# Kernel tuning notes

Hardware: AMD Instinct MI355X
Metric: run time of the kernel (lower is better)

Reference implementation:

```python
import jax, jax.numpy as jnp
import numpy as np

EPS = 1e-12
N_HEADS = 16


def _ln(x, g, b, eps=EPS):
    m = jnp.mean(x, axis=-1, keepdims=True)
    v = jnp.var(x, axis=-1, keepdims=True)
    return (x - m) * jax.lax.rsqrt(v + eps) * g + b


def setup_inputs() -> dict:
    key = jax.random.key(0)
    ks = jax.random.split(key, 8)
    B, S, D, I = 2, 2048, 1024, 4096
    s = 0.02
    f32 = jnp.float32
    return {
        "x": jax.random.normal(ks[0], (B, S, D), f32),
        "input_mask": jnp.zeros((B, 1, 1, S), f32),  # additive mask, 0 = no masking
        "norm_w": jnp.ones((D,), f32),
        "norm_b": jnp.zeros((D,), f32),
        "attn_qkvw": jax.random.normal(ks[1], (D, 3 * D), f32) * s,
        "attn_qkvb": jnp.zeros((3 * D,), f32),
        "attn_ow": jax.random.normal(ks[2], (D, D), f32) * s,
        "attn_ob": jnp.zeros((D,), f32),
        "attn_nw": jnp.ones((D,), f32),
        "attn_nb": jnp.zeros((D,), f32),
        "inter_w": jax.random.normal(ks[3], (D, I), f32) * s,
        "inter_b": jnp.zeros((I,), f32),
        "inter_w1": jax.random.normal(ks[4], (D, I), f32) * s,
        "output_w": jax.random.normal(ks[5], (I, D), f32) * s,
        "output_b": jnp.zeros((D,), f32),
    }


def reference(x, input_mask, norm_w, norm_b, attn_qkvw, attn_qkvb, attn_ow,
              attn_ob, attn_nw, attn_nb, inter_w, inter_b, inter_w1,
              output_w, output_b):
    B, S, D = x.shape
    hd = D // N_HEADS

    # --- fused qkv_gemm: pre-layernorm + QKV GEMM + bias ---
    ln1 = _ln(x, norm_w, norm_b)
    qkv = ln1 @ attn_qkvw + attn_qkvb            # [B,S,3D]
    q, k, v = jnp.split(qkv, 3, axis=-1)

    def to_heads(t):  # [B,S,D] -> [B,H,S,hd]
        return t.reshape(B, S, N_HEADS, hd).transpose(0, 2, 1, 3)

    q, k, v = to_heads(q), to_heads(k), to_heads(v)

    # --- softmax-context attention (scale_attention=True -> 1/sqrt(head_dim)) ---
    scores = jnp.einsum('bhqd,bhkd->bhqk', q, k) / jnp.sqrt(jnp.float32(hd))
    scores = scores + input_mask                 # additive mask [B,1,1,S]
    probs = jax.nn.softmax(scores, axis=-1)
    ctx = jnp.einsum('bhqk,bhkd->bhqd', probs, v)
    ctx = ctx.transpose(0, 2, 1, 3).reshape(B, S, D)

    attn_out = ctx @ attn_ow                     # vector_matmul (no bias)

    # --- fused mlp_gemm: bias+residual add, layernorm, GEMM+bias+gelu ---
    residual_add = attn_out + attn_ob + x
    ln2 = _ln(residual_add, attn_nw, attn_nb)
    intermediate = jax.nn.gelu(ln2 @ inter_w + inter_b, approximate=False)
    # gated path: vector_matmul(mlp input, inter_w1) * intermediate (per source)
    intermediate = (attn_out @ inter_w1) * intermediate

    # --- output projection + bias_residual ---
    out = intermediate @ output_w + output_b + residual_add
    return out
```

## Files before the change

kernel.cpp:

```cpp
#include <hip/hip_runtime.h>
#include <hip/hip_bf16.h>

#define BATCH 2
#define SEQ   2048
#define DIM   1024
#define IDIM  4096
#define NH    16
#define HD    64
#define TOK   (BATCH * SEQ)

typedef __hip_bfloat16 bf16;

typedef short bf16x8_t __attribute__((ext_vector_type(8)));
typedef float f32x4_t  __attribute__((ext_vector_type(4)));

__device__ __forceinline__ float ldv(const float* p, size_t i) { return p[i]; }
__device__ __forceinline__ float ldv(const bf16*  p, size_t i) { return __bfloat162float(p[i]); }
__device__ __forceinline__ void  stv(float* p, size_t i, float v) { p[i] = v; }
__device__ __forceinline__ void  stv(bf16*  p, size_t i, float v) { p[i] = __float2bfloat16(v); }

__device__ __forceinline__ f32x4_t mfma16(bf16x8_t a, bf16x8_t b, f32x4_t c) {
    return __builtin_amdgcn_mfma_f32_16x16x32_bf16(a, b, c, 0, 0, 0);
}

__device__ __forceinline__ void gload16(const bf16* g, bf16* l) {
    __builtin_amdgcn_global_load_lds(
        (const __attribute__((address_space(1))) void*)g,
        (__attribute__((address_space(3))) void*)l, 16, 0, 0);
}

__device__ __forceinline__ void xcd_map(int &bx, int &by) {
    const int gn  = gridDim.x;
    const int lin = blockIdx.y * gn + blockIdx.x;
    const int cx  = gn >> 3;
    const int xcd = lin & 7;
    const int slot = lin >> 3;
    bx = xcd * cx + slot % cx;
    by = slot / cx;
}

__device__ __forceinline__ void ln_one_row(const float* __restrict__ in,
                                           const float* __restrict__ w,
                                           const float* __restrict__ b,
                                           bf16* __restrict__ out,
                                           int row, int lane) {
    const float4* xr = (const float4*)(in + (size_t)row * DIM);
    float4 v[4];
    float sum = 0.f, sq = 0.f;
#pragma unroll
    for (int i = 0; i < 4; i++) {
        v[i] = xr[lane + i * 64];
        sum += v[i].x + v[i].y + v[i].z + v[i].w;
        sq  += v[i].x * v[i].x + v[i].y * v[i].y + v[i].z * v[i].z + v[i].w * v[i].w;
    }
#pragma unroll
    for (int off = 32; off >= 1; off >>= 1) {
        sum += __shfl_xor(sum, off);
        sq  += __shfl_xor(sq,  off);
    }
    const float mean = sum * (1.f / DIM);
    const float var  = fmaxf(sq * (1.f / DIM) - mean * mean, 0.f);
    const float rstd = rsqrtf(var + 1e-12f);

    const float4* wv = (const float4*)w;
    const float4* bv = (const float4*)b;
    ushort4* orow = (ushort4*)(out + (size_t)row * DIM);
#pragma unroll
    for (int i = 0; i < 4; i++) {
        const int c = lane + i * 64;
        const float4 wc = wv[c];
        const float4 bc = bv[c];
        ushort4 o;
        o.x = __bfloat16_as_ushort(__float2bfloat16((v[i].x - mean) * rstd * wc.x + bc.x));
        o.y = __bfloat16_as_ushort(__float2bfloat16((v[i].y - mean) * rstd * wc.y + bc.y));
        o.z = __bfloat16_as_ushort(__float2bfloat16((v[i].z - mean) * rstd * wc.z + bc.z));
        o.w = __bfloat16_as_ushort(__float2bfloat16((v[i].w - mean) * rstd * wc.w + bc.w));
        orow[c] = o;
    }
}

__global__ __launch_bounds__(256) void ln_kernel(const float* __restrict__ in,
                                                 const float* __restrict__ w,
                                                 const float* __restrict__ b,
                                                 bf16* __restrict__ out) {
    ln_one_row(in, w, b, out, blockIdx.x * 4 + (threadIdx.x >> 6), threadIdx.x & 63);
}

__global__ __launch_bounds__(256) void wconv5ln_kernel(
        const float* __restrict__ W0, bf16* __restrict__ T0,
        const float* __restrict__ W1, bf16* __restrict__ T1,
        const float* __restrict__ W2, bf16* __restrict__ T2,
        const float* __restrict__ W3, bf16* __restrict__ T3,
        const float* __restrict__ W4, bf16* __restrict__ T4,
        const float* __restrict__ x, const float* __restrict__ nw,
        const float* __restrict__ nb, bf16* __restrict__ lnout) {
    __shared__ float tile[32][33];
    int bid = blockIdx.x;
    if (bid >= 16384) {
        ln_one_row(x, nw, nb, lnout,
                   (bid - 16384) * 4 + (threadIdx.x >> 6), threadIdx.x & 63);
        return;
    }
    const float* W; bf16* T; int K, N;
    if (bid < 3072)       { W = W0; T = T0; K = 1024; N = 3072; }
    else if (bid < 4096)  { W = W1; T = T1; K = 1024; N = 1024; bid -= 3072; }
    else if (bid < 8192)  { W = W2; T = T2; K = 1024; N = 4096; bid -= 4096; }
    else if (bid < 12288) { W = W3; T = T3; K = 1024; N = 4096; bid -= 8192; }
    else                  { W = W4; T = T4; K = 4096; N = 1024; bid -= 12288; }
    const int ntx = N >> 5;
    const int n0 = (bid % ntx) * 32;
    const int k0 = (bid / ntx) * 32;

    const int tid = threadIdx.x;
    const int c = tid & 31;
    const int r = tid >> 5;
#pragma unroll
    for (int i = 0; i < 4; i++)
        tile[r + i * 8][c] = W[(size_t)(k0 + r + i * 8) * N + n0 + c];
    __syncthreads();
#pragma unroll
    for (int i = 0; i < 4; i++)
        T[(size_t)(n0 + r + i * 8) * K + k0 + c] = __float2bfloat16(tile[c][r + i * 8]);
}

#define GBK 32

template<typename TX, int MODE, int TM, int TN>
__global__ __launch_bounds__(256) void mgemm_kernel(const bf16* __restrict__ A,
                                                    const bf16* __restrict__ Bt,
                                                    const float* __restrict__ bias,
                                                    const TX* __restrict__ aux,
                                                    TX* __restrict__ C,
                                                    const float* __restrict__ bias2,
                                                    const float* __restrict__ xin,
                                                    float* __restrict__ C2,
                                                    int M, int N, int K) {
    constexpr int TILE_M = TM * 32;
    constexpr int TILE_N = TN * 32;
    constexpr int LOADS  = TM / 2 + TN / 2;
    __shared__ alignas(16) bf16 As[2][TILE_M][GBK];
    __shared__ alignas(16) bf16 Bs[2][TILE_N][GBK];

    const int tid  = threadIdx.x;
    const int w    = tid >> 6;
    const int lane = tid & 63;
    const int cl   = lane & 15;
    const int qd   = lane >> 4;
    const int wm   = w >> 1;
    const int wn   = w & 1;

    int bx, by;
    xcd_map(bx, by);

    const int row0 = by * TILE_M;
    const int col0 = bx * TILE_N;

    const int lrow = lane >> 2;
    const int lkg  = lane & 3;
    const int sslot = lkg ^ ((lrow >> 1) & 3);
    const int rds   = (cl >> 1) & 3;

    const bf16* gA = A  + (size_t)(row0 + lrow) * K + sslot * 8;
    const bf16* gB = Bt + (size_t)(col0 + lrow) * K + sslot * 8;

    f32x4_t acc[TM][TN];
#pragma unroll
    for (int m = 0; m < TM; m++)
#pragma unroll
        for (int n = 0; n < TN; n++) acc[m][n] = {0.f, 0.f, 0.f, 0.f};

    auto stage = [&](int b, int k0) {
#pragma unroll
        for (int i = 0; i < TM / 2; i++) {
            const int r16 = (w * (TM / 2) + i) * 16;
            gload16(gA + (size_t)r16 * K + k0, &As[b][r16][0]);
        }
#pragma unroll
        for (int j = 0; j < TN / 2; j++) {
            const int r16 = (w * (TN / 2) + j) * 16;
            gload16(gB + (size_t)r16 * K + k0, &Bs[b][r16][0]);
        }
    };

    stage(0, 0);
    stage(1, GBK);
    asm volatile("s_waitcnt vmcnt(%0)" :: "i"(LOADS) : "memory");
    __builtin_amdgcn_s_barrier();

    const int NT = K / GBK;
    for (int t = 0; t < NT; t++) {
        const int cur = t & 1;

        bf16x8_t af[TM], bfr[TN];
#pragma unroll
        for (int m = 0; m < TM; m++)
            af[m] = *(const bf16x8_t*)&As[cur][wm * (TM * 16) + m * 16 + cl][(qd ^ rds) * 8];
#pragma unroll
        for (int n = 0; n < TN; n++)
            bfr[n] = *(const bf16x8_t*)&Bs[cur][wn * (TN * 16) + n * 16 + cl][(qd ^ rds) * 8];
        asm volatile("s_waitcnt lgkmcnt(0)" ::: "memory");
        __builtin_amdgcn_sched_barrier(0);
        __builtin_amdgcn_s_barrier();

        if (t + 2 < NT) stage(cur, (t + 2) * GBK);

        __builtin_amdgcn_s_setprio(1);
#pragma unroll
        for (int m = 0; m < TM; m++)
#pragma unroll
            for (int n = 0; n < TN; n++)
                acc[m][n] = mfma16(af[m], bfr[n], acc[m][n]);
        __builtin_amdgcn_s_setprio(0);

        if (t + 1 < NT) {
            if (t + 2 < NT)
                asm volatile("s_waitcnt vmcnt(%0)" :: "i"(LOADS) : "memory");
            else
                asm volatile("s_waitcnt vmcnt(0)" ::: "memory");
            __builtin_amdgcn_s_barrier();
        }
    }

#pragma unroll
    for (int m = 0; m < TM; m++) {
#pragma unroll
        for (int n = 0; n < TN; n++) {
            const int gc = col0 + wn * (TN * 16) + n * 16 + cl;
            const float bv = (MODE != 4 && bias) ? bias[gc] : 0.f;
#pragma unroll
            for (int r = 0; r < 4; r++) {
                const int gr = row0 + wm * (TM * 16) + m * 16 + qd * 4 + r;
                float c = acc[m][n][r] + bv;
                if (MODE == 3) {
                    c += ldv(aux, (size_t)gr * N + gc);
                }
                stv(C, (size_t)gr * N + gc, c);
                if (MODE == 4) {
                    C2[(size_t)gr * N + gc] = c + bias2[gc] + xin[(size_t)gr * N + gc];
                }
            }
        }
    }
}

__global__ __launch_bounds__(512, 4) void dualgemm_kernel(const bf16* __restrict__ A0,
                                                          const bf16* __restrict__ B0t,
                                                          const bf16* __restrict__ A1,
                                                          const bf16* __restrict__ B1t,
                                                          const float* __restrict__ bias,
                                                          bf16* __restrict__ C,
                                                          int M, int N, int K) {
    __shared__ alignas(16) char pool[66560];

    const int tid  = threadIdx.x;
    const int w    = tid >> 6;
    const int lane = tid & 63;
    const int cl   = lane & 15;
    const int qd   = lane >> 4;
    const int gsel = w >> 2;
    const int g2   = w & 3;
    const int wm   = g2 >> 1;
    const int wn   = g2 & 1;

    int bx, by;
    xcd_map(bx, by);
    const int row0 = by * 128;
    const int col0 = bx * 128;

    const int lrow = lane >> 2;
    const int lkg  = lane & 3;
    const int sslot = lkg ^ ((lrow >> 1) & 3);
    const int rds   = (cl >> 1) & 3;

    const int sarr = w >> 1;
    const bf16* gsrc;
    {
        const bf16* bases[4] = {A0, B0t, A1, B1t};
        const int   r0s[4]   = {row0, col0, row0, col0};
        gsrc = bases[sarr] + (size_t)(r0s[sarr] + lrow) * K + sslot * 8;
    }

    auto sptr = [&](int b, int a) -> bf16* {
        return (bf16*)(pool + b * 32768 + a * 8192);
    };

    f32x4_t acc[4][4];
#pragma unroll
    for (int m = 0; m < 4; m++)
#pragma unroll
        for (int n = 0; n < 4; n++) acc[m][n] = {0.f, 0.f, 0.f, 0.f};

    auto stage = [&](int b, int k0) {
        bf16* dst = sptr(b, sarr);
#pragma unroll
        for (int j = 0; j < 4; j++) {
            const int rg = (w & 1) * 4 + j;
            gload16(gsrc + (size_t)(rg * 16) * K + k0, dst + rg * 16 * GBK);
        }
    };

    stage(0, 0);
    stage(1, GBK);
    asm volatile("s_waitcnt vmcnt(4)" ::: "memory");
    __builtin_amdgcn_s_barrier();

    const int NT = K / GBK;
    for (int t = 0; t < NT; t++) {
        const int cur = t & 1;
        const bf16* Sa = sptr(cur, gsel * 2);
        const bf16* Sb = sptr(cur, gsel * 2 + 1);

        bf16x8_t af[4], bfr[4];
#pragma unroll
        for (int m = 0; m < 4; m++)
            af[m] = *(const bf16x8_t*)&Sa[(wm * 64 + m * 16 + cl) * GBK + (qd ^ rds) * 8];
#pragma unroll
        for (int n = 0; n < 4; n++)
            bfr[n] = *(const bf16x8_t*)&Sb[(wn * 64 + n * 16 + cl) * GBK + (qd ^ rds) * 8];
        asm volatile("s_waitcnt lgkmcnt(0)" ::: "memory");
        __builtin_amdgcn_sched_barrier(0);
        __builtin_amdgcn_s_barrier();

        if (t + 2 < NT) stage(cur, (t + 2) * GBK);

        __builtin_amdgcn_s_setprio(1);
#pragma unroll
        for (int m = 0; m < 4; m++)
#pragma unroll
            for (int n = 0; n < 4; n++)
                acc[m][n] = mfma16(af[m], bfr[n], acc[m][n]);
        __builtin_amdgcn_s_setprio(0);

        if (t + 1 < NT) {
            if (t + 2 < NT)
                asm volatile("s_waitcnt vmcnt(4)" ::: "memory");
            else
                asm volatile("s_waitcnt vmcnt(0)" ::: "memory");
            __builtin_amdgcn_s_barrier();
        }
    }

    float* X = (float*)pool;
    __syncthreads();
    if (gsel == 1) {
#pragma unroll
        for (int m = 0; m < 4; m++)
#pragma unroll
            for (int n = 0; n < 4; n++)
#pragma unroll
                for (int r = 0; r < 4; r++)
                    X[(wm * 64 + m * 16 + qd * 4 + r) * 130 + wn * 64 + n * 16 + cl] =
                        acc[m][n][r];
    }
    __syncthreads();
    if (gsel == 0) {
#pragma unroll
        for (int m = 0; m < 4; m++) {
#pragma unroll
            for (int n = 0; n < 4; n++) {
                const int lc = wn * 64 + n * 16 + cl;
                const int gc = col0 + lc;
                const float bv = bias[gc];
#pragma unroll
                for (int r = 0; r < 4; r++) {
                    const int lr = wm * 64 + m * 16 + qd * 4 + r;
                    float g = acc[m][n][r] + bv;
                    g = 0.5f * g * (1.f + erff(g * 0.70710678118654752f));
                    C[(size_t)(row0 + lr) * N + gc] = __float2bfloat16(g * X[lr * 130 + lc]);
                }
            }
        }
    }
}

__global__ __launch_bounds__(256) void vtrans_kernel(const bf16* __restrict__ qkv,
                                                     bf16* __restrict__ vt) {
    __shared__ bf16 t[64][72];
    const int tid = threadIdx.x;
    const int s0  = blockIdx.x * 64;
    const int bh  = blockIdx.y;
    const int bb  = bh >> 4;
    const int h   = bh & 15;
    const bf16* src = qkv + (size_t)bb * SEQ * (3 * DIM) + 2 * DIM + h * HD;
    const int r  = tid >> 3;
    const int cc = tid & 7;
#pragma unroll
    for (int i = 0; i < 2; i++)
        *(bf16x8_t*)&t[r + i * 32][cc * 8] =
            *(const bf16x8_t*)(src + (size_t)(s0 + r + i * 32) * (3 * DIM) + cc * 8);
    __syncthreads();
    bf16* dst = vt + (size_t)bh * HD * SEQ + s0;
#pragma unroll
    for (int i = 0; i < 2; i++) {
        const int d = r + i * 32;
        bf16x8_t v;
#pragma unroll
        for (int j = 0; j < 8; j++)
            ((short*)&v)[j] = *(const short*)&t[cc * 8 + j][d];
        *(bf16x8_t*)(dst + (size_t)d * SEQ + cc * 8) = v;
    }
}

#define KCH 64
#define NCH (SEQ / KCH)

__device__ __forceinline__ unsigned pk2(float lo, float hi) {
    unsigned a = (unsigned)__bfloat16_as_ushort(__float2bfloat16(lo));
    unsigned b = (unsigned)__bfloat16_as_ushort(__float2bfloat16(hi));
    return a | (b << 16);
}

union PAU { bf16x8_t v; unsigned u[4]; };

__global__ __launch_bounds__(256, 2) void attn_mfma_kernel(const bf16* __restrict__ qkv,
                                                           const bf16* __restrict__ vt,
                                                           const float* __restrict__ mask,
                                                           bf16* __restrict__ ctx) {
    __shared__ alignas(16) bf16 Kl[2][KCH][64];
    __shared__ alignas(16) bf16 Vl[2][KCH][64];

    const int tid  = threadIdx.x;
    const int w    = tid >> 6;
    const int lane = tid & 63;
    const int cl   = lane & 15;
    const int qd   = lane >> 4;
    const int c7   = cl & 7;

    const int qtile = blockIdx.x;
    const int bh    = blockIdx.y;
    const int bb    = bh >> 4;
    const int h     = bh & 15;

    const bf16*  base = qkv + (size_t)bb * SEQ * (3 * DIM) + h * HD;
    const bf16*  gK   = base + DIM;
    const bf16*  gV   = vt + (size_t)bh * HD * SEQ;
    const float* mrow = mask + (size_t)bb * SEQ;

    bf16x8_t aq[2][2];
#pragma unroll
    for (int qt = 0; qt < 2; qt++) {
        const bf16* qrow = base + (size_t)(qtile * 128 + w * 32 + qt * 16 + cl) * (3 * DIM);
        aq[qt][0] = *(const bf16x8_t*)(qrow + qd * 8);
        aq[qt][1] = *(const bf16x8_t*)(qrow + 32 + qd * 8);
    }

    const bf16x8_t onesv = {0x3F80, 0x3F80, 0x3F80, 0x3F80,
                            0x3F80, 0x3F80, 0x3F80, 0x3F80};

    const int sr  = lane >> 3;
    const int scw = (lane & 7) ^ sr;

#pragma unroll
    for (int i = 0; i < 2; i++) {
        const int row = i * 32 + w * 8 + sr;
        gload16(gK + (size_t)row * (3 * DIM) + scw * 8, &Kl[0][i * 32 + w * 8][0]);
        gload16(gV + (size_t)row * SEQ + scw * 8, &Vl[0][i * 32 + w * 8][0]);
    }
    f32x4_t mkx[4];
#pragma unroll
    for (int ks = 0; ks < 4; ks++)
        mkx[ks] = *(const f32x4_t*)&mrow[ks * 16 + qd * 4];

    f32x4_t O[2][4];
#pragma unroll
    for (int qt = 0; qt < 2; qt++)
#pragma unroll
        for (int ns = 0; ns < 4; ns++) O[qt][ns] = {0.f, 0.f, 0.f, 0.f};
    f32x4_t li[2] = {{0.f,0.f,0.f,0.f},{0.f,0.f,0.f,0.f}};

    for (int c = 0; c < NCH; c++) {
        __syncthreads();
        const bf16 (*Kb)[64] = Kl[c & 1];
        const bf16 (*Vb)[64] = Vl[c & 1];

        f32x4_t mk[4];
#pragma unroll
        for (int ks = 0; ks < 4; ks++) mk[ks] = mkx[ks];

        if (c + 1 < NCH) {
            bf16 (*Kn)[64] = Kl[(c + 1) & 1];
            bf16 (*Vn)[64] = Vl[(c + 1) & 1];
            const int k0n = (c + 1) * KCH;
#pragma unroll
            for (int i = 0; i < 2; i++) {
                const int row = i * 32 + w * 8 + sr;
                gload16(gK + (size_t)(k0n + row) * (3 * DIM) + scw * 8, &Kn[i * 32 + w * 8][0]);
                gload16(gV + (size_t)row * SEQ + k0n + scw * 8, &Vn[i * 32 + w * 8][0]);
            }
#pragma unroll
            for (int ks = 0; ks < 4; ks++)
                mkx[ks] = *(const f32x4_t*)&mrow[k0n + ks * 16 + qd * 4];
        }

        bf16x8_t kf[4][2];
#pragma unroll
        for (int ks = 0; ks < 4; ks++) {
            kf[ks][0] = *(const bf16x8_t*)&Kb[ks * 16 + cl][(qd ^ c7) << 3];
            kf[ks][1] = *(const bf16x8_t*)&Kb[ks * 16 + cl][((4 + qd) ^ c7) << 3];
        }

        PAU pa[2][2];
#pragma unroll
        for (int qt = 0; qt < 2; qt++) {
            unsigned Dv[4][2];
#pragma unroll
            for (int ks = 0; ks < 4; ks++) {
                f32x4_t s = {0.f, 0.f, 0.f, 0.f};
                s = mfma16(kf[ks][0], aq[qt][0], s);
                s = mfma16(kf[ks][1], aq[qt][1], s);
                const float e0 = __expf(s[0] * 0.125f + mk[ks][0]);
                const float e1 = __expf(s[1] * 0.125f + mk[ks][1]);
                const float e2 = __expf(s[2] * 0.125f + mk[ks][2]);
                const float e3 = __expf(s[3] * 0.125f + mk[ks][3]);
                Dv[ks][0] = pk2(e0, e1);
                Dv[ks][1] = pk2(e2, e3);
            }
#pragma unroll
            for (int rp = 0; rp < 2; rp++) {
                auto z0 = __builtin_amdgcn_permlane32_swap(Dv[0][rp], Dv[1][rp], false, false);
                auto w0 = __builtin_amdgcn_permlane16_swap(z0[0], z0[1], false, false);
                pa[qt][0].u[rp]     = w0[0];
                pa[qt][0].u[rp + 2] = w0[1];
                auto z1 = __builtin_amdgcn_permlane32_swap(Dv[2][rp], Dv[3][rp], false, false);
                auto w1 = __builtin_amdgcn_permlane16_swap(z1[0], z1[1], false, false);
                pa[qt][1].u[rp]     = w1[0];
                pa[qt][1].u[rp + 2] = w1[1];
            }
            f32x4_t ls = {0.f, 0.f, 0.f, 0.f};
            ls = mfma16(pa[qt][0].v, onesv, ls);
            ls = mfma16(pa[qt][1].v, onesv, ls);
            li[qt] += ls;
        }

#pragma unroll
        for (int ns = 0; ns < 4; ns++) {
            bf16x8_t v0 = *(const bf16x8_t*)&Vb[ns * 16 + cl][(qd ^ c7) << 3];
            bf16x8_t v1 = *(const bf16x8_t*)&Vb[ns * 16 + cl][((4 + qd) ^ c7) << 3];
#pragma unroll
            for (int qt = 0; qt < 2; qt++) {
                O[qt][ns] = mfma16(pa[qt][0].v, v0, O[qt][ns]);
                O[qt][ns] = mfma16(pa[qt][1].v, v1, O[qt][ns]);
            }
        }
    }

#pragma unroll
    for (int qt = 0; qt < 2; qt++) {
#pragma unroll
        for (int r = 0; r < 4; r++) {
            const int row = qtile * 128 + w * 32 + qt * 16 + qd * 4 + r;
            bf16* orow = ctx + (size_t)(bb * SEQ + row) * DIM + h * HD;
            const float inv = 1.f / li[qt][r];
#pragma unroll
            for (int ns = 0; ns < 4; ns++)
                orow[ns * 16 + cl] = __float2bfloat16(O[qt][ns][r] * inv);
        }
    }
}

extern "C" void kernel_launch(void* const* d_in, const int* in_sizes, int n_in,
                              void* d_out, int out_size, void* d_ws, size_t ws_size,
                              hipStream_t stream) {
    const float* x        = (const float*)d_in[0];
    const float* mask     = (const float*)d_in[1];
    const float* norm_w   = (const float*)d_in[2];
    const float* norm_b   = (const float*)d_in[3];
    const float* qkvw     = (const float*)d_in[4];
    const float* qkvb     = (const float*)d_in[5];
    const float* attn_ow  = (const float*)d_in[6];
    const float* attn_ob  = (const float*)d_in[7];
    const float* attn_nw  = (const float*)d_in[8];
    const float* attn_nb  = (const float*)d_in[9];
    const float* inter_w  = (const float*)d_in[10];
    const float* inter_b  = (const float*)d_in[11];
    const float* inter_w1 = (const float*)d_in[12];
    const float* output_w = (const float*)d_in[13];
    const float* output_b = (const float*)d_in[14];

    float* out = (float*)d_out;
    bf16*  ws  = (bf16*)d_ws;

    const size_t M1 = 1024 * 1024;
    bf16* ln_s      = ws;
    bf16* qkv       = ws + 4 * M1;
    bf16* inter     = ws + 4 * M1;
    bf16* qkvw_t    = ws + 16 * M1;
    bf16* attn_owt  = ws + 19 * M1;
    bf16* vt        = ws + 20 * M1;
    bf16* attn_out  = ws + 20 * M1;
    bf16* inter_wt  = ws + 24 * M1;
    bf16* inter_w1t = ws + 28 * M1;
    bf16* output_wt = ws + 32 * M1;
    float* resid    = out;

    dim3 blk(256);
    dim3 blk512(512);

    wconv5ln_kernel<<<dim3(16384 + TOK / 4), blk, 0, stream>>>(
        qkvw, qkvw_t, attn_ow, attn_owt, inter_w, inter_wt,
        inter_w1, inter_w1t, output_w, output_wt,
        x, norm_w, norm_b, ln_s);

    mgemm_kernel<bf16, 0, 4, 4><<<dim3(3072 / 128, TOK / 128), blk, 0, stream>>>(
        ln_s, qkvw_t, qkvb, (const bf16*)nullptr, qkv,
        nullptr, nullptr, nullptr, TOK, 3 * DIM, DIM);

    vtrans_kernel<<<dim3(SEQ / 64, BATCH * NH), blk, 0, stream>>>(qkv, vt);

    attn_mfma_kernel<<<dim3(SEQ / 128, BATCH * NH), blk, 0, stream>>>(qkv, vt, mask, ln_s);

    mgemm_kernel<bf16, 4, 4, 2><<<dim3(DIM / 64, TOK / 128), blk, 0, stream>>>(
        ln_s, attn_owt, (const float*)nullptr, (const bf16*)nullptr, attn_out,
        attn_ob, x, resid, TOK, DIM, DIM);

    ln_kernel<<<TOK / 4, blk, 0, stream>>>(resid, attn_nw, attn_nb, ln_s);

    dualgemm_kernel<<<dim3(IDIM / 128, TOK / 128), blk512, 0, stream>>>(
        ln_s, inter_wt, attn_out, inter_w1t, inter_b, inter, TOK, IDIM, DIM);

    mgemm_kernel<float, 3, 4, 2><<<dim3(DIM / 64, TOK / 128), blk, 0, stream>>>(
        inter, output_wt, output_b, resid, out,
        nullptr, nullptr, nullptr, TOK, DIM, IDIM);
}
```

Baseline: 434.3 us.

## Split attention query tile across eight waves with one 16-row subtile each

The attention kernel now launches 512 threads per block, and each of the eight waves handles 16 query rows instead of 32. Each thread issues one K/V chunk load per iteration instead of two. This halves per-wave register state (O accumulators, Q fragments) and raises occupancy to hide exp/MFMA latency. In exchange, each wave re-reads the full K and V fragments from LDS for half the work, which doubles LDS read traffic per useful MFMA and adds barrier cost across more waves.

```diff
diff --git a/kernel.cpp b/kernel.cpp
--- a/kernel.cpp
+++ b/kernel.cpp
@@ -412,7 +412,7 @@
 
 union PAU { bf16x8_t v; unsigned u[4]; };
 
-__global__ __launch_bounds__(256, 2) void attn_mfma_kernel(const bf16* __restrict__ qkv,
+__global__ __launch_bounds__(512, 4) void attn_mfma_kernel(const bf16* __restrict__ qkv,
                                                            const bf16* __restrict__ vt,
                                                            const float* __restrict__ mask,
                                                            bf16* __restrict__ ctx) {
@@ -436,13 +436,9 @@
     const bf16*  gV   = vt + (size_t)bh * HD * SEQ;
     const float* mrow = mask + (size_t)bb * SEQ;
 
-    bf16x8_t aq[2][2];
-#pragma unroll
-    for (int qt = 0; qt < 2; qt++) {
-        const bf16* qrow = base + (size_t)(qtile * 128 + w * 32 + qt * 16 + cl) * (3 * DIM);
-        aq[qt][0] = *(const bf16x8_t*)(qrow + qd * 8);
-        aq[qt][1] = *(const bf16x8_t*)(qrow + 32 + qd * 8);
-    }
+    const bf16* qrow = base + (size_t)(qtile * 128 + w * 16 + cl) * (3 * DIM);
+    const bf16x8_t aq0 = *(const bf16x8_t*)(qrow + qd * 8);
+    const bf16x8_t aq1 = *(const bf16x8_t*)(qrow + 32 + qd * 8);
 
     const bf16x8_t onesv = {0x3F80, 0x3F80, 0x3F80, 0x3F80,
                             0x3F80, 0x3F80, 0x3F80, 0x3F80};
@@ -450,23 +446,18 @@
     const int sr  = lane >> 3;
     const int scw = (lane & 7) ^ sr;
 
-#pragma unroll
-    for (int i = 0; i < 2; i++) {
-        const int row = i * 32 + w * 8 + sr;
-        gload16(gK + (size_t)row * (3 * DIM) + scw * 8, &Kl[0][i * 32 + w * 8][0]);
-        gload16(gV + (size_t)row * SEQ + scw * 8, &Vl[0][i * 32 + w * 8][0]);
+    {
+        const int row = w * 8 + sr;
+        gload16(gK + (size_t)row * (3 * DIM) + scw * 8, &Kl[0][w * 8][0]);
+        gload16(gV + (size_t)row * SEQ + scw * 8, &Vl[0][w * 8][0]);
     }
     f32x4_t mkx[4];
 #pragma unroll
     for (int ks = 0; ks < 4; ks++)
         mkx[ks] = *(const f32x4_t*)&mrow[ks * 16 + qd * 4];
 
-    f32x4_t O[2][4];
-#pragma unroll
-    for (int qt = 0; qt < 2; qt++)
-#pragma unroll
-        for (int ns = 0; ns < 4; ns++) O[qt][ns] = {0.f, 0.f, 0.f, 0.f};
-    f32x4_t li[2] = {{0.f,0.f,0.f,0.f},{0.f,0.f,0.f,0.f}};
+    f32x4_t O[4] = {{0,0,0,0},{0,0,0,0},{0,0,0,0},{0,0,0,0}};
+    f32x4_t li = {0.f, 0.f, 0.f, 0.f};
 
     for (int c = 0; c < NCH; c++) {
         __syncthreads();
@@ -481,12 +472,9 @@
             bf16 (*Kn)[64] = Kl[(c + 1) & 1];
             bf16 (*Vn)[64] = Vl[(c + 1) & 1];
             const int k0n = (c + 1) * KCH;
-#pragma unroll
-            for (int i = 0; i < 2; i++) {
-                const int row = i * 32 + w * 8 + sr;
-                gload16(gK + (size_t)(k0n + row) * (3 * DIM) + scw * 8, &Kn[i * 32 + w * 8][0]);
-                gload16(gV + (size_t)row * SEQ + k0n + scw * 8, &Vn[i * 32 + w * 8][0]);
-            }
+            const int row = w * 8 + sr;
+            gload16(gK + (size_t)(k0n + row) * (3 * DIM) + scw * 8, &Kn[w * 8][0]);
+            gload16(gV + (size_t)row * SEQ + k0n + scw * 8, &Vn[w * 8][0]);
 #pragma unroll
             for (int ks = 0; ks < 4; ks++)
                 mkx[ks] = *(const f32x4_t*)&mrow[k0n + ks * 16 + qd * 4];
@@ -499,62 +487,53 @@
             kf[ks][1] = *(const bf16x8_t*)&Kb[ks * 16 + cl][((4 + qd) ^ c7) << 3];
         }
 
-        PAU pa[2][2];
-#pragma unroll
-        for (int qt = 0; qt < 2; qt++) {
-            unsigned Dv[4][2];
-#pragma unroll
-            for (int ks = 0; ks < 4; ks++) {
-                f32x4_t s = {0.f, 0.f, 0.f, 0.f};
-                s = mfma16(kf[ks][0], aq[qt][0], s);
-                s = mfma16(kf[ks][1], aq[qt][1], s);
-                const float e0 = __expf(s[0] * 0.125f + mk[ks][0]);
-                const float e1 = __expf(s[1] * 0.125f + mk[ks][1]);
-                const float e2 = __expf(s[2] * 0.125f + mk[ks][2]);
-                const float e3 = __expf(s[3] * 0.125f + mk[ks][3]);
-                Dv[ks][0] = pk2(e0, e1);
-                Dv[ks][1] = pk2(e2, e3);
-            }
-#pragma unroll
-            for (int rp = 0; rp < 2; rp++) {
-                auto z0 = __builtin_amdgcn_permlane32_swap(Dv[0][rp], Dv[1][rp], false, false);
-                auto w0 = __builtin_amdgcn_permlane16_swap(z0[0], z0[1], false, false);
-                pa[qt][0].u[rp]     = w0[0];
-                pa[qt][0].u[rp + 2] = w0[1];
-                auto z1 = __builtin_amdgcn_permlane32_swap(Dv[2][rp], Dv[3][rp], false, false);
-                auto w1 = __builtin_amdgcn_permlane16_swap(z1[0], z1[1], false, false);
-                pa[qt][1].u[rp]     = w1[0];
-                pa[qt][1].u[rp + 2] = w1[1];
-            }
-            f32x4_t ls = {0.f, 0.f, 0.f, 0.f};
-            ls = mfma16(pa[qt][0].v, onesv, ls);
-            ls = mfma16(pa[qt][1].v, onesv, ls);
-            li[qt] += ls;
-        }
+        unsigned Dv[4][2];
+#pragma unroll
+        for (int ks = 0; ks < 4; ks++) {
+            f32x4_t s = {0.f, 0.f, 0.f, 0.f};
+            s = mfma16(kf[ks][0], aq0, s);
+            s = mfma16(kf[ks][1], aq1, s);
+            const float e0 = __expf(s[0] * 0.125f + mk[ks][0]);
+            const float e1 = __expf(s[1] * 0.125f + mk[ks][1]);
+            const float e2 = __expf(s[2] * 0.125f + mk[ks][2]);
+            const float e3 = __expf(s[3] * 0.125f + mk[ks][3]);
+            Dv[ks][0] = pk2(e0, e1);
+            Dv[ks][1] = pk2(e2, e3);
+        }
+        PAU pa0, pa1;
+#pragma unroll
+        for (int rp = 0; rp < 2; rp++) {
+            auto z0 = __builtin_amdgcn_permlane32_swap(Dv[0][rp], Dv[1][rp], false, false);
+            auto w0 = __builtin_amdgcn_permlane16_swap(z0[0], z0[1], false, false);
+            pa0.u[rp]     = w0[0];
+            pa0.u[rp + 2] = w0[1];
+            auto z1 = __builtin_amdgcn_permlane32_swap(Dv[2][rp], Dv[3][rp], false, false);
+            auto w1 = __builtin_amdgcn_permlane16_swap(z1[0], z1[1], false, false);
+            pa1.u[rp]     = w1[0];
+            pa1.u[rp + 2] = w1[1];
+        }
+        f32x4_t ls = {0.f, 0.f, 0.f, 0.f};
+        ls = mfma16(pa0.v, onesv, ls);
+        ls = mfma16(pa1.v, onesv, ls);
+        li += ls;
 
 #pragma unroll
         for (int ns = 0; ns < 4; ns++) {
             bf16x8_t v0 = *(const bf16x8_t*)&Vb[ns * 16 + cl][(qd ^ c7) << 3];
             bf16x8_t v1 = *(const bf16x8_t*)&Vb[ns * 16 + cl][((4 + qd) ^ c7) << 3];
-#pragma unroll
-            for (int qt = 0; qt < 2; qt++) {
-                O[qt][ns] = mfma16(pa[qt][0].v, v0, O[qt][ns]);
-                O[qt][ns] = mfma16(pa[qt][1].v, v1, O[qt][ns]);
-            }
-        }
-    }
-
-#pragma unroll
-    for (int qt = 0; qt < 2; qt++) {
-#pragma unroll
-        for (int r = 0; r < 4; r++) {
-            const int row = qtile * 128 + w * 32 + qt * 16 + qd * 4 + r;
-            bf16* orow = ctx + (size_t)(bb * SEQ + row) * DIM + h * HD;
-            const float inv = 1.f / li[qt][r];
-#pragma unroll
-            for (int ns = 0; ns < 4; ns++)
-                orow[ns * 16 + cl] = __float2bfloat16(O[qt][ns][r] * inv);
-        }
+            O[ns] = mfma16(pa0.v, v0, O[ns]);
+            O[ns] = mfma16(pa1.v, v1, O[ns]);
+        }
+    }
+
+#pragma unroll
+    for (int r = 0; r < 4; r++) {
+        const int row = qtile * 128 + w * 16 + qd * 4 + r;
+        bf16* orow = ctx + (size_t)(bb * SEQ + row) * DIM + h * HD;
+        const float inv = 1.f / li[r];
+#pragma unroll
+        for (int ns = 0; ns < 4; ns++)
+            orow[ns * 16 + cl] = __float2bfloat16(O[ns][r] * inv);
     }
 }
 
@@ -607,7 +586,7 @@
 
     vtrans_kernel<<<dim3(SEQ / 64, BATCH * NH), blk, 0, stream>>>(qkv, vt);
 
-    attn_mfma_kernel<<<dim3(SEQ / 128, BATCH * NH), blk, 0, stream>>>(qkv, vt, mask, ln_s);
+    attn_mfma_kernel<<<dim3(SEQ / 128, BATCH * NH), blk512, 0, stream>>>(qkv, vt, mask, ln_s);
 
     mgemm_kernel<bf16, 4, 4, 2><<<dim3(DIM / 64, TOK / 128), blk, 0, stream>>>(
         ln_s, attn_owt, (const float*)nullptr, (const bf16*)nullptr, attn_out,
```

Result: no change. 428.9 us, median of 2 (-1.2%).
